# Performance work log

Measured on AMD Instinct MI355X. Metric: run time of the kernel, lower is better.

## Reference

```python
import jax, jax.numpy as jnp
import numpy as np

N_USER = 200000
N_ITEM = 100000
N = N_USER + N_ITEM
D = 64
NNZ = 1250000
B = 4096
N_LAYERS = 3


def setup_inputs() -> dict:
    key = jax.random.key(0)
    ks = jax.random.split(key, 7)
    user_emb = jax.random.normal(ks[0], (N_USER, D), dtype=jnp.float32) * 0.1
    item_emb = jax.random.normal(ks[1], (N_ITEM, D), dtype=jnp.float32) * 0.1
    # normalized-adjacency-like values (D^-1/2 A D^-1/2 entries are small positive)
    adj_val = jax.random.uniform(ks[2], (NNZ,), dtype=jnp.float32) * 0.1
    adj_row = jax.random.randint(ks[3], (NNZ,), 0, N, dtype=jnp.int32)
    adj_col = jax.random.randint(ks[4], (NNZ,), 0, N, dtype=jnp.int32)
    users = jax.random.randint(ks[5], (B,), 0, N_USER, dtype=jnp.int64)
    items = jax.random.randint(ks[6], (B,), 0, N_ITEM, dtype=jnp.int64)
    return {"user_emb": user_emb, "item_emb": item_emb, "adj_val": adj_val,
            "adj_row": adj_row, "adj_col": adj_col, "users": users, "items": items}


def reference(user_emb, item_emb, adj_val, adj_row, adj_col, users, items):
    # computer(): repeated SpMM propagation + mean over layer embeddings
    all_emb = jnp.concatenate([user_emb, item_emb], axis=0)  # [N, D]
    emb = all_emb
    acc = all_emb  # running sum of per-layer embeddings (fused stack+mean)
    for _ in range(N_LAYERS):
        # SpMM: out[r] += val * emb[c] for each edge (r, c)
        gathered = emb[adj_col] * adj_val[:, None]          # [NNZ, D]
        emb = jax.ops.segment_sum(gathered, adj_row, num_segments=N)
        acc = acc + emb
    light_out = acc / (N_LAYERS + 1)                        # mean over L+1 layers
    users_emb = light_out[users]                            # [B, D]
    items_emb = light_out[N_USER + items]                   # [B, D]
    # forward(): sigmoid(U @ I^T)
    return jax.nn.sigmoid(jnp.einsum('bd,cd->bc', users_emb, items_emb))
```

## Files before the change

### kernel.cpp

```cpp
#include <hip/hip_runtime.h>

#define N_USER 200000
#define N_ITEM 100000
#define NN     (N_USER + N_ITEM)
#define D      64
#define NNZ    1250000
#define B      4096

#define CHUNK  4096
#define NCHK   ((NNZ + CHUNK - 1) / CHUNK)
#define NBKT   ((NN + 1023) >> 10)
#define CAP    5000

#define VAL_SCALE   81920.0f
#define VAL_INV     (1.0f / 81920.0f)

typedef __attribute__((ext_vector_type(8))) short  short8;
typedef __attribute__((ext_vector_type(4))) float  f32x4;

__device__ __forceinline__ unsigned f2bf(float f) {
    unsigned u = __float_as_uint(f);
    return (u + 0x7fffu + ((u >> 16) & 1u)) >> 16;
}
__device__ __forceinline__ unsigned pack2(float lo, float hi) {
    return f2bf(lo) | (f2bf(hi) << 16);
}
__device__ __forceinline__ float bflo(unsigned u) { return __uint_as_float(u << 16); }
__device__ __forceinline__ float bfhi(unsigned u) { return __uint_as_float(u & 0xffff0000u); }

__global__ __launch_bounds__(256) void k_ui_init(const float4* __restrict__ user_emb,
                                                 const float4* __restrict__ item_emb,
                                                 const int* __restrict__ users,
                                                 const int* __restrict__ items,
                                                 float4* __restrict__ U,
                                                 float4* __restrict__ I) {
    int idx = blockIdx.x * 256 + threadIdx.x;
    if (idx >= 2 * B * 16) return;
    if (idx < B * 16) {
        int b = idx >> 4, q = idx & 15;
        U[idx] = user_emb[users[b] * 16 + q];
    } else {
        int j = idx - B * 16;
        int b = j >> 4, q = j & 15;
        I[j] = item_emb[items[b] * 16 + q];
    }
}

__global__ __launch_bounds__(256) void k_bhist(const int* __restrict__ adj_row,
                                               int* __restrict__ cntG) {
    __shared__ int c[NBKT];
    int t = threadIdx.x;
    for (int i = t; i < NBKT; i += 256) c[i] = 0;
    __syncthreads();
    int base = blockIdx.x * CHUNK;
    int n = min(CHUNK, NNZ - base);
    for (int i = t; i < n; i += 256) atomicAdd(&c[adj_row[base + i] >> 10], 1);
    __syncthreads();
    for (int i = t; i < NBKT; i += 256)
        if (c[i]) atomicAdd(&cntG[i], c[i]);
}

__global__ __launch_bounds__(512) void k_bscan(const int* __restrict__ cntG,
                                               int* __restrict__ bases,
                                               int* __restrict__ cursor,
                                               int* __restrict__ ptr) {
    __shared__ int s[512];
    int t = threadIdx.x;
    int v = (t < NBKT) ? cntG[t] : 0;
    s[t] = v;
    __syncthreads();
    for (int off = 1; off < 512; off <<= 1) {
        int x = (t >= off) ? s[t - off] : 0;
        __syncthreads();
        s[t] += x;
        __syncthreads();
    }
    if (t < NBKT) { bases[t] = s[t] - v; cursor[t] = s[t] - v; }
    if (t == 0) ptr[NN] = NNZ;
}

__global__ __launch_bounds__(256) void k_bin(const int* __restrict__ adj_row,
                                             const int* __restrict__ adj_col,
                                             const float* __restrict__ adj_val,
                                             int* __restrict__ cursor,
                                             uint2* __restrict__ binned) {
    __shared__ int cnt[NBKT], exc[NBKT], gof[NBKT], cur[NBKT];
    __shared__ int s[512];
    __shared__ uint2 stg[CHUNK];
    int t = threadIdx.x;
    int base = blockIdx.x * CHUNK;
    int n = min(CHUNK, NNZ - base);

    for (int i = t; i < NBKT; i += 256) cnt[i] = 0;
    __syncthreads();
    for (int i = t; i < n; i += 256) atomicAdd(&cnt[adj_row[base + i] >> 10], 1);
    __syncthreads();

    s[t]       = (t < NBKT) ? cnt[t] : 0;
    s[t + 256] = (t + 256 < NBKT) ? cnt[t + 256] : 0;
    __syncthreads();
    for (int off = 1; off < 512; off <<= 1) {
        int a  = (t >= off) ? s[t - off] : 0;
        int b2 = (t + 256 >= off) ? s[t + 256 - off] : 0;
        __syncthreads();
        s[t] += a; s[t + 256] += b2;
        __syncthreads();
    }
    for (int i = t; i < NBKT; i += 256) {
        int e = s[i] - cnt[i];
        exc[i] = e;
        cur[i] = e;
        gof[i] = cnt[i] ? atomicAdd(&cursor[i], cnt[i]) : 0;
    }
    __syncthreads();

    for (int i = t; i < n; i += 256) {
        int row = adj_row[base + i];
        int b2 = row >> 10;
        unsigned q = (unsigned)__float2int_rn(adj_val[base + i] * VAL_SCALE);
        if (q > 8191u) q = 8191u;
        unsigned cv = ((unsigned)adj_col[base + i] << 13) | q;
        int p = atomicAdd(&cur[b2], 1);
        stg[p] = make_uint2(cv, (unsigned)row);
    }
    __syncthreads();

    for (int i = t; i < n; i += 256) {
        uint2 e = stg[i];
        int b2 = (int)(e.y >> 10);
        binned[gof[b2] + (i - exc[b2])] = e;
    }
}

__global__ __launch_bounds__(1024) void k_fine(const int* __restrict__ bases,
                                               const int* __restrict__ cursor,
                                               const uint2* __restrict__ binned,
                                               int* __restrict__ ptr,
                                               unsigned* __restrict__ packed) {
    __shared__ int hist[1024], scn[1024];
    __shared__ unsigned img[CAP];
    int t = threadIdx.x;
    int b = blockIdx.x;
    int ebeg = bases[b], eend = cursor[b];
    int n = eend - ebeg;

    hist[t] = 0;
    __syncthreads();
    for (int i = t; i < n; i += 1024)
        atomicAdd(&hist[binned[ebeg + i].y & 1023], 1);
    __syncthreads();

    scn[t] = hist[t];
    __syncthreads();
    for (int off = 1; off < 1024; off <<= 1) {
        int a = (t >= off) ? scn[t - off] : 0;
        __syncthreads();
        scn[t] += a;
        __syncthreads();
    }
    int exc = scn[t] - hist[t];
    int row = (b << 10) + t;
    if (row < NN) ptr[row] = ebeg + exc;
    __syncthreads();
    scn[t] = exc;
    __syncthreads();

    for (int i = t; i < n; i += 1024) {
        uint2 e = binned[ebeg + i];
        int p = atomicAdd(&scn[e.y & 1023], 1);
        img[p] = e.x;
    }
    __syncthreads();
    for (int i = t; i < n; i += 1024) packed[ebeg + i] = img[i];
}

__global__ __launch_bounds__(256) void k_mark3(const int* __restrict__ users,
                                               const int* __restrict__ items,
                                               const int* __restrict__ ptr,
                                               const unsigned* __restrict__ packed,
                                               int* __restrict__ flags2,
                                               int* __restrict__ flags1) {
    int i = blockIdx.x * 256 + threadIdx.x;
    if (i >= 2 * B) return;
    int node = (i < B) ? users[i] : N_USER + items[i - B];
    flags2[node] = 1;
    flags1[node] = 1;
    int beg = ptr[node], end = ptr[node + 1];
    for (int e = beg; e < end; e++) flags2[(int)(packed[e] >> 13)] = 1;
}

__global__ __launch_bounds__(256) void k_mark2(const int* __restrict__ list2,
                                               const int* __restrict__ pn2,
                                               const int* __restrict__ ptr,
                                               const unsigned* __restrict__ packed,
                                               int* __restrict__ flags1) {
    int i = blockIdx.x * 256 + threadIdx.x;
    if (i >= pn2[0]) return;
    int row = list2[i];
    int beg = ptr[row], end = ptr[row + 1];
    for (int e = beg; e < end; e++) flags1[(int)(packed[e] >> 13)] = 1;
}

__global__ __launch_bounds__(256) void k_fcnt(const int* __restrict__ flags,
                                              int* __restrict__ cnts) {
    __shared__ int s[256];
    int t = threadIdx.x;
    int base = blockIdx.x * 1024 + t * 4;
    int c = 0;
#pragma unroll
    for (int i = 0; i < 4; i++) {
        int idx = base + i;
        if (idx < NN) c += flags[idx];
    }
    s[t] = c;
    __syncthreads();
    for (int off = 128; off > 0; off >>= 1) {
        if (t < off) s[t] += s[t + off];
        __syncthreads();
    }
    if (t == 0) cnts[blockIdx.x] = s[0];
}

__global__ __launch_bounds__(512) void k_fscan(const int* __restrict__ cnts,
                                               int* __restrict__ cbase,
                                               int* __restrict__ pn) {
    __shared__ int s[512];
    int t = threadIdx.x;
    int v = (t < NBKT) ? cnts[t] : 0;
    s[t] = v;
    __syncthreads();
    for (int off = 1; off < 512; off <<= 1) {
        int x = (t >= off) ? s[t - off] : 0;
        __syncthreads();
        s[t] += x;
        __syncthreads();
    }
    if (t < NBKT) cbase[t] = s[t] - v;
    if (t == 511) pn[0] = s[511];
}

__global__ __launch_bounds__(256) void k_fscat(const int* __restrict__ flags,
                                               const int* __restrict__ cbase,
                                               int* __restrict__ list) {
    __shared__ int s[256];
    int t = threadIdx.x;
    int base = blockIdx.x * 1024 + t * 4;
    int f[4];
    int c = 0;
#pragma unroll
    for (int i = 0; i < 4; i++) {
        int idx = base + i;
        f[i] = (idx < NN) ? flags[idx] : 0;
        c += f[i];
    }
    s[t] = c;
    __syncthreads();
    for (int off = 1; off < 256; off <<= 1) {
        int x = (t >= off) ? s[t - off] : 0;
        __syncthreads();
        s[t] += x;
        __syncthreads();
    }
    int run = cbase[blockIdx.x] + s[t] - c;
#pragma unroll
    for (int i = 0; i < 4; i++) {
        if (f[i]) list[run++] = base + i;
    }
}

template <bool L0>
__global__ __launch_bounds__(256) void k_spmm_list(const int* __restrict__ ptr,
                                                   const unsigned* __restrict__ packed,
                                                   const int* __restrict__ list,
                                                   const int* __restrict__ pn,
                                                   const float4* __restrict__ ue,
                                                   const float4* __restrict__ ie,
                                                   const uint4* __restrict__ ecur,
                                                   uint4* __restrict__ enext) {
    int t = blockIdx.x * 256 + threadIdx.x;
    int ir = t >> 3;
    if (ir >= pn[0]) return;
    int row = list[ir], q = t & 7;
    int beg = ptr[row], end = ptr[row + 1];
    float acc[8] = {};
    for (int i = beg; i < end; i++) {
        unsigned w = packed[i];
        int col = (int)(w >> 13);
        float val = (float)(w & 8191u) * VAL_INV;
        if (L0) {
            const float4* src = (col < N_USER) ? (ue + (size_t)col * 16)
                                               : (ie + (size_t)(col - N_USER) * 16);
            float4 a = src[q * 2];
            float4 b = src[q * 2 + 1];
            acc[0] += val * a.x; acc[1] += val * a.y;
            acc[2] += val * a.z; acc[3] += val * a.w;
            acc[4] += val * b.x; acc[5] += val * b.y;
            acc[6] += val * b.z; acc[7] += val * b.w;
        } else {
            uint4 u = ecur[(size_t)col * 8 + q];
            acc[0] += val * bflo(u.x); acc[1] += val * bfhi(u.x);
            acc[2] += val * bflo(u.y); acc[3] += val * bfhi(u.y);
            acc[4] += val * bflo(u.z); acc[5] += val * bfhi(u.z);
            acc[6] += val * bflo(u.w); acc[7] += val * bfhi(u.w);
        }
    }
    uint4 o;
    o.x = pack2(acc[0], acc[1]);
    o.y = pack2(acc[2], acc[3]);
    o.z = pack2(acc[4], acc[5]);
    o.w = pack2(acc[6], acc[7]);
    enext[(size_t)row * 8 + q] = o;
}

__global__ __launch_bounds__(256) void k_spmm_final(const int* __restrict__ ptr,
                                                    const unsigned* __restrict__ packed,
                                                    const int* __restrict__ users,
                                                    const int* __restrict__ items,
                                                    const uint4* __restrict__ ecur,
                                                    float4* __restrict__ U,
                                                    float4* __restrict__ I) {
    int idx = blockIdx.x * 256 + threadIdx.x;
    if (idx >= 2 * B * 8) return;
    int b = idx >> 3, q = idx & 7;
    int node;
    float4* dst;
    if (b < B) { node = users[b]; dst = U + idx * 2; }
    else       { node = N_USER + items[b - B]; dst = I + (idx - B * 8) * 2; }
    int beg = ptr[node], end = ptr[node + 1];
    float acc[8] = {};
    for (int i = beg; i < end; i++) {
        unsigned w = packed[i];
        int col = (int)(w >> 13);
        float val = (float)(w & 8191u) * VAL_INV;
        uint4 u = ecur[(size_t)col * 8 + q];
        acc[0] += val * bflo(u.x); acc[1] += val * bfhi(u.x);
        acc[2] += val * bflo(u.y); acc[3] += val * bfhi(u.y);
        acc[4] += val * bflo(u.z); acc[5] += val * bfhi(u.z);
        acc[6] += val * bflo(u.w); acc[7] += val * bfhi(u.w);
    }
    float4 lo = dst[0], hi = dst[1];
    lo.x += acc[0]; lo.y += acc[1]; lo.z += acc[2]; lo.w += acc[3];
    hi.x += acc[4]; hi.y += acc[5]; hi.z += acc[6]; hi.w += acc[7];
    dst[0] = lo; dst[1] = hi;
}

__global__ __launch_bounds__(256) void k_gather(const uint4* __restrict__ enext,
                                                const int* __restrict__ users,
                                                const int* __restrict__ items,
                                                float4* __restrict__ U,
                                                float4* __restrict__ I) {
    int idx = blockIdx.x * 256 + threadIdx.x;
    if (idx >= 2 * B * 8) return;
    int node;
    float4* dst;
    if (idx < B * 8) {
        int b = idx >> 3;
        node = users[b];
        dst = U + idx * 2;
    } else {
        int j = idx - B * 8;
        int b = j >> 3;
        node = N_USER + items[b];
        dst = I + j * 2;
    }
    int q = idx & 7;
    uint4 u = enext[(size_t)node * 8 + q];
    float4 lo = dst[0], hi = dst[1];
    lo.x += bflo(u.x); lo.y += bfhi(u.x);
    lo.z += bflo(u.y); lo.w += bfhi(u.y);
    hi.x += bflo(u.z); hi.y += bfhi(u.z);
    hi.z += bflo(u.w); hi.w += bfhi(u.w);
    dst[0] = lo; dst[1] = hi;
}

__global__ __launch_bounds__(256) void k_cvt(const float4* __restrict__ U,
                                             const float4* __restrict__ I,
                                             uint4* __restrict__ ubi) {
    int idx = blockIdx.x * 256 + threadIdx.x;
    if (idx >= 2 * B * 8) return;
    const float4* src = (idx < B * 8) ? (U + idx * 2) : (I + (idx - B * 8) * 2);
    float4 a = src[0], b = src[1];
    uint4 o;
    o.x = pack2(a.x, a.y);
    o.y = pack2(a.z, a.w);
    o.z = pack2(b.x, b.y);
    o.w = pack2(b.z, b.w);
    ubi[idx] = o;
}

__global__ __launch_bounds__(256) void k_gemm_mfma(const short8* __restrict__ ubi,
                                                   float* __restrict__ out) {
    __shared__ float lds[4 * 64 * 32];
    int t = threadIdx.x;
    int lane = t & 63;
    int w = t >> 6;
    int bx = blockIdx.x & 63;
    int by = blockIdx.x >> 6;
    int wm = (w >> 1) * 64;
    int wn = (w & 1) * 32;

    int r16  = lane & 15;
    int kg   = lane >> 4;

    short8 a[4][2], b[2][2];
#pragma unroll
    for (int mi = 0; mi < 4; mi++) {
        int row = by * 128 + wm + mi * 16 + r16;
#pragma unroll
        for (int kk = 0; kk < 2; kk++)
            a[mi][kk] = ubi[row * 8 + kk * 4 + kg];
    }
#pragma unroll
    for (int ni = 0; ni < 2; ni++) {
        int row = B + bx * 64 + wn + ni * 16 + r16;
#pragma unroll
        for (int kk = 0; kk < 2; kk++)
            b[ni][kk] = ubi[row * 8 + kk * 4 + kg];
    }

    f32x4 acc[4][2] = {};
#pragma unroll
    for (int mi = 0; mi < 4; mi++)
#pragma unroll
        for (int ni = 0; ni < 2; ni++) {
            acc[mi][ni] = __builtin_amdgcn_mfma_f32_16x16x32_bf16(
                a[mi][0], b[ni][0], acc[mi][ni], 0, 0, 0);
            acc[mi][ni] = __builtin_amdgcn_mfma_f32_16x16x32_bf16(
                a[mi][1], b[ni][1], acc[mi][ni], 0, 0, 0);
        }

    const float s = 1.0f / 16.0f;
    float* wls = lds + w * (64 * 32);
#pragma unroll
    for (int mi = 0; mi < 4; mi++) {
#pragma unroll
        for (int ni = 0; ni < 2; ni++) {
            int c  = ni * 16 + r16;
            int c4 = c >> 2, cl = c & 3;
#pragma unroll
            for (int r = 0; r < 4; r++) {
                int rr = mi * 16 + kg * 4 + r;
                float v = 1.0f / (1.0f + __expf(-acc[mi][ni][r] * s));
                wls[rr * 32 + (((c4 ^ (rr & 7)) << 2) | cl)] = v;
            }
        }
    }

    float4* out4 = (float4*)out;
    int j = lane & 7;
    int i0 = lane >> 3;
    size_t colbase = (size_t)(bx * 16) + (w & 1) * 8 + j;
#pragma unroll
    for (int iter = 0; iter < 8; iter++) {
        int i = iter * 8 + i0;
        float4 vv = *(float4*)&wls[i * 32 + ((j ^ (i & 7)) << 2)];
        out4[(size_t)(by * 128 + wm + i) * 1024 + colbase] = vv;
    }
}

extern "C" void kernel_launch(void* const* d_in, const int* in_sizes, int n_in,
                              void* d_out, int out_size, void* d_ws, size_t ws_size,
                              hipStream_t stream) {
    const float* user_emb = (const float*)d_in[0];
    const float* item_emb = (const float*)d_in[1];
    const float* adj_val  = (const float*)d_in[2];
    const int*   adj_row  = (const int*)d_in[3];
    const int*   adj_col  = (const int*)d_in[4];
    const int*   users    = (const int*)d_in[5];
    const int*   items    = (const int*)d_in[6];
    float* out = (float*)d_out;

    unsigned short* embA = (unsigned short*)d_ws;
    unsigned short* embB = embA + (size_t)NN * D;
    float* U    = (float*)(embB + (size_t)NN * D);
    float* I    = U + (size_t)B * D;
    int*   ptr  = (int*)(I + (size_t)B * D);
    unsigned* packed = (unsigned*)(ptr + (NN + 4));
    uint2* binned = (uint2*)(packed + NNZ);
    int*   cntG   = (int*)(binned + NNZ);
    int*   bases  = cntG + 512;
    int*   cursor = bases + 512;
    int*   cnts   = cursor + 512;
    int*   cbase  = cnts + 512;
    int*   pn     = cbase + 512;
    int*   flags2 = pn + 8;
    int*   flags1 = flags2 + NN;
    int*   list2  = flags1 + NN;
    int*   list1  = list2 + NN;
    unsigned short* ubi = (unsigned short*)(list1 + NN);

    k_ui_init<<<(2 * B * 16 + 255) / 256, 256, 0, stream>>>(
        (const float4*)user_emb, (const float4*)item_emb,
        users, items, (float4*)U, (float4*)I);

    hipMemsetAsync(cntG, 0, 512 * 4, stream);
    k_bhist<<<NCHK, 256, 0, stream>>>(adj_row, cntG);
    k_bscan<<<1, 512, 0, stream>>>(cntG, bases, cursor, ptr);
    k_bin<<<NCHK, 256, 0, stream>>>(adj_row, adj_col, adj_val, cursor, binned);
    k_fine<<<NBKT, 1024, 0, stream>>>(bases, cursor, binned, ptr, packed);

    hipMemsetAsync(flags2, 0, (size_t)2 * NN * 4, stream);
    k_mark3<<<(2 * B + 255) / 256, 256, 0, stream>>>(
        users, items, ptr, packed, flags2, flags1);
    k_fcnt<<<NBKT, 256, 0, stream>>>(flags2, cnts);
    k_fscan<<<1, 512, 0, stream>>>(cnts, cbase, &pn[0]);
    k_fscat<<<NBKT, 256, 0, stream>>>(flags2, cbase, list2);
    k_mark2<<<(NN + 255) / 256, 256, 0, stream>>>(list2, &pn[0], ptr, packed, flags1);
    k_fcnt<<<NBKT, 256, 0, stream>>>(flags1, cnts);
    k_fscan<<<1, 512, 0, stream>>>(cnts, cbase, &pn[1]);
    k_fscat<<<NBKT, 256, 0, stream>>>(flags1, cbase, list1);

    const int spmmGrid = (NN * 8 + 255) / 256;
    const int gatGrid  = (2 * B * 8 + 255) / 256;

    k_spmm_list<true><<<spmmGrid, 256, 0, stream>>>(
        ptr, packed, list1, &pn[1],
        (const float4*)user_emb, (const float4*)item_emb,
        (const uint4*)embA, (uint4*)embA);
    k_gather<<<gatGrid, 256, 0, stream>>>(
        (const uint4*)embA, users, items, (float4*)U, (float4*)I);

    k_spmm_list<false><<<spmmGrid, 256, 0, stream>>>(
        ptr, packed, list2, &pn[0],
        (const float4*)user_emb, (const float4*)item_emb,
        (const uint4*)embA, (uint4*)embB);
    k_gather<<<gatGrid, 256, 0, stream>>>(
        (const uint4*)embB, users, items, (float4*)U, (float4*)I);

    k_spmm_final<<<gatGrid, 256, 0, stream>>>(
        ptr, packed, users, items, (const uint4*)embB, (float4*)U, (float4*)I);

    k_cvt<<<(2 * B * 8 + 255) / 256, 256, 0, stream>>>(
        (const float4*)U, (const float4*)I, (uint4*)ubi);
    k_gemm_mfma<<<2048, 256, 0, stream>>>((const short8*)ubi, out);
}
```

Baseline: 159.3 us.

## Mark reachable rows on COO first and build CSR only for needed rows

Reachability marking (seed nodes, then two hops) now runs directly on the COO edge list with byte flags, before the CSR is built. Histogramming and binning then keep only edges whose row is in the two-hop set, which shrinks the binned and packed arrays. The flag count/scan/scatter kernels are replaced by atomic list compaction fused into the bucket-scan kernel. The gather, accumulate and convert kernels are merged into one finalize kernel. Layer 0 gets a 16-lane SpMM reading fp32 inputs, and the GEMM is split into two launches with nontemporal output stores. The price is two extra full passes over the edges and list ordering that depends on atomics.

```diff
diff --git a/kernel.cpp b/kernel.cpp
--- a/kernel.cpp
+++ b/kernel.cpp
@@ -15,6 +15,7 @@
 #define VAL_SCALE   81920.0f
 #define VAL_INV     (1.0f / 81920.0f)
 
+typedef unsigned char u8;
 typedef __attribute__((ext_vector_type(8))) short  short8;
 typedef __attribute__((ext_vector_type(4))) float  f32x4;
 
@@ -28,25 +29,30 @@
 __device__ __forceinline__ float bflo(unsigned u) { return __uint_as_float(u << 16); }
 __device__ __forceinline__ float bfhi(unsigned u) { return __uint_as_float(u & 0xffff0000u); }
 
-__global__ __launch_bounds__(256) void k_ui_init(const float4* __restrict__ user_emb,
-                                                 const float4* __restrict__ item_emb,
-                                                 const int* __restrict__ users,
-                                                 const int* __restrict__ items,
-                                                 float4* __restrict__ U,
-                                                 float4* __restrict__ I) {
-    int idx = blockIdx.x * 256 + threadIdx.x;
-    if (idx >= 2 * B * 16) return;
-    if (idx < B * 16) {
-        int b = idx >> 4, q = idx & 15;
-        U[idx] = user_emb[users[b] * 16 + q];
-    } else {
-        int j = idx - B * 16;
-        int b = j >> 4, q = j & 15;
-        I[j] = item_emb[items[b] * 16 + q];
-    }
+__global__ __launch_bounds__(256) void k_mark_sel(const int* __restrict__ users,
+                                                  const int* __restrict__ items,
+                                                  u8* __restrict__ flagS,
+                                                  u8* __restrict__ flag2,
+                                                  u8* __restrict__ flag1) {
+    int i = blockIdx.x * 256 + threadIdx.x;
+    if (i >= 2 * B) return;
+    int node = (i < B) ? users[i] : N_USER + items[i - B];
+    flagS[node] = 1;
+    flag2[node] = 1;
+    flag1[node] = 1;
+}
+
+__global__ __launch_bounds__(256) void k_markstep(const int* __restrict__ adj_row,
+                                                  const int* __restrict__ adj_col,
+                                                  const u8* __restrict__ flagIn,
+                                                  u8* __restrict__ flagOut) {
+    int e = blockIdx.x * 256 + threadIdx.x;
+    if (e >= NNZ) return;
+    if (flagIn[adj_row[e]]) flagOut[adj_col[e]] = 1;
 }
 
 __global__ __launch_bounds__(256) void k_bhist(const int* __restrict__ adj_row,
+                                               const u8* __restrict__ flag1,
                                                int* __restrict__ cntG) {
     __shared__ int c[NBKT];
     int t = threadIdx.x;
@@ -54,38 +60,59 @@
     __syncthreads();
     int base = blockIdx.x * CHUNK;
     int n = min(CHUNK, NNZ - base);
-    for (int i = t; i < n; i += 256) atomicAdd(&c[adj_row[base + i] >> 10], 1);
+    for (int i = t; i < n; i += 256) {
+        int r = adj_row[base + i];
+        if (flag1[r]) atomicAdd(&c[r >> 10], 1);
+    }
     __syncthreads();
     for (int i = t; i < NBKT; i += 256)
         if (c[i]) atomicAdd(&cntG[i], c[i]);
 }
 
-__global__ __launch_bounds__(512) void k_bscan(const int* __restrict__ cntG,
-                                               int* __restrict__ bases,
-                                               int* __restrict__ cursor,
-                                               int* __restrict__ ptr) {
-    __shared__ int s[512];
+__global__ __launch_bounds__(512) void k_scan_compact(const int* __restrict__ cntG,
+                                                      int* __restrict__ bases,
+                                                      int* __restrict__ cursor,
+                                                      int* __restrict__ ptr,
+                                                      const u8* __restrict__ flag2,
+                                                      const u8* __restrict__ flag1,
+                                                      int* __restrict__ list2,
+                                                      int* __restrict__ list1,
+                                                      int* __restrict__ pn) {
     int t = threadIdx.x;
-    int v = (t < NBKT) ? cntG[t] : 0;
-    s[t] = v;
-    __syncthreads();
-    for (int off = 1; off < 512; off <<= 1) {
-        int x = (t >= off) ? s[t - off] : 0;
+    if (blockIdx.x == 0) {
+        __shared__ int s[512];
+        int v = (t < NBKT) ? cntG[t] : 0;
+        s[t] = v;
         __syncthreads();
-        s[t] += x;
-        __syncthreads();
-    }
-    if (t < NBKT) { bases[t] = s[t] - v; cursor[t] = s[t] - v; }
-    if (t == 0) ptr[NN] = NNZ;
+        for (int off = 1; off < 512; off <<= 1) {
+            int x = (t >= off) ? s[t - off] : 0;
+            __syncthreads();
+            s[t] += x;
+            __syncthreads();
+        }
+        if (t < NBKT) { bases[t] = s[t] - v; cursor[t] = s[t] - v; }
+        if (t == NBKT - 1) ptr[NN] = s[t];
+    }
+    int base = blockIdx.x * 1024;
+#pragma unroll
+    for (int k = 0; k < 2; k++) {
+        int i = base + k * 512 + t;
+        if (i < NN) {
+            if (flag2[i]) list2[atomicAdd(&pn[0], 1)] = i;
+            if (flag1[i]) list1[atomicAdd(&pn[1], 1)] = i;
+        }
+    }
 }
 
 __global__ __launch_bounds__(256) void k_bin(const int* __restrict__ adj_row,
                                              const int* __restrict__ adj_col,
                                              const float* __restrict__ adj_val,
+                                             const u8* __restrict__ flag1,
                                              int* __restrict__ cursor,
                                              uint2* __restrict__ binned) {
     __shared__ int cnt[NBKT], exc[NBKT], gof[NBKT], cur[NBKT];
     __shared__ int s[512];
+    __shared__ int tot;
     __shared__ uint2 stg[CHUNK];
     int t = threadIdx.x;
     int base = blockIdx.x * CHUNK;
@@ -93,7 +120,10 @@
 
     for (int i = t; i < NBKT; i += 256) cnt[i] = 0;
     __syncthreads();
-    for (int i = t; i < n; i += 256) atomicAdd(&cnt[adj_row[base + i] >> 10], 1);
+    for (int i = t; i < n; i += 256) {
+        int r = adj_row[base + i];
+        if (flag1[r]) atomicAdd(&cnt[r >> 10], 1);
+    }
     __syncthreads();
 
     s[t]       = (t < NBKT) ? cnt[t] : 0;
@@ -112,20 +142,21 @@
         cur[i] = e;
         gof[i] = cnt[i] ? atomicAdd(&cursor[i], cnt[i]) : 0;
     }
+    if (t == 0) tot = s[NBKT - 1];
     __syncthreads();
 
     for (int i = t; i < n; i += 256) {
         int row = adj_row[base + i];
-        int b2 = row >> 10;
+        if (!flag1[row]) continue;
         unsigned q = (unsigned)__float2int_rn(adj_val[base + i] * VAL_SCALE);
         if (q > 8191u) q = 8191u;
         unsigned cv = ((unsigned)adj_col[base + i] << 13) | q;
-        int p = atomicAdd(&cur[b2], 1);
+        int p = atomicAdd(&cur[row >> 10], 1);
         stg[p] = make_uint2(cv, (unsigned)row);
     }
     __syncthreads();
 
-    for (int i = t; i < n; i += 256) {
+    for (int i = t; i < tot; i += 256) {
         uint2 e = stg[i];
         int b2 = (int)(e.y >> 10);
         binned[gof[b2] + (i - exc[b2])] = e;
@@ -174,109 +205,39 @@
     for (int i = t; i < n; i += 1024) packed[ebeg + i] = img[i];
 }
 
-__global__ __launch_bounds__(256) void k_mark3(const int* __restrict__ users,
-                                               const int* __restrict__ items,
-                                               const int* __restrict__ ptr,
+__global__ __launch_bounds__(256) void k_spmm16(const int* __restrict__ ptr,
+                                                const unsigned* __restrict__ packed,
+                                                const int* __restrict__ list,
+                                                const int* __restrict__ pn,
+                                                const float4* __restrict__ ue,
+                                                const float4* __restrict__ ie,
+                                                uint2* __restrict__ enext) {
+    int t = blockIdx.x * 256 + threadIdx.x;
+    int ir = t >> 4;
+    if (ir >= pn[1]) return;
+    int row = list[ir], q = t & 15;
+    int beg = ptr[row], end = ptr[row + 1];
+    float a0 = 0.f, a1 = 0.f, a2 = 0.f, a3 = 0.f;
+    for (int i = beg; i < end; i++) {
+        unsigned w = packed[i];
+        int col = (int)(w >> 13);
+        float val = (float)(w & 8191u) * VAL_INV;
+        float4 v = (col < N_USER) ? ue[(size_t)col * 16 + q]
+                                  : ie[(size_t)(col - N_USER) * 16 + q];
+        a0 += val * v.x; a1 += val * v.y; a2 += val * v.z; a3 += val * v.w;
+    }
+    uint2 o;
+    o.x = pack2(a0, a1);
+    o.y = pack2(a2, a3);
+    enext[(size_t)row * 16 + q] = o;
+}
+
+__global__ __launch_bounds__(256) void k_spmm8(const int* __restrict__ ptr,
                                                const unsigned* __restrict__ packed,
-                                               int* __restrict__ flags2,
-                                               int* __restrict__ flags1) {
-    int i = blockIdx.x * 256 + threadIdx.x;
-    if (i >= 2 * B) return;
-    int node = (i < B) ? users[i] : N_USER + items[i - B];
-    flags2[node] = 1;
-    flags1[node] = 1;
-    int beg = ptr[node], end = ptr[node + 1];
-    for (int e = beg; e < end; e++) flags2[(int)(packed[e] >> 13)] = 1;
-}
-
-__global__ __launch_bounds__(256) void k_mark2(const int* __restrict__ list2,
-                                               const int* __restrict__ pn2,
-                                               const int* __restrict__ ptr,
-                                               const unsigned* __restrict__ packed,
-                                               int* __restrict__ flags1) {
-    int i = blockIdx.x * 256 + threadIdx.x;
-    if (i >= pn2[0]) return;
-    int row = list2[i];
-    int beg = ptr[row], end = ptr[row + 1];
-    for (int e = beg; e < end; e++) flags1[(int)(packed[e] >> 13)] = 1;
-}
-
-__global__ __launch_bounds__(256) void k_fcnt(const int* __restrict__ flags,
-                                              int* __restrict__ cnts) {
-    __shared__ int s[256];
-    int t = threadIdx.x;
-    int base = blockIdx.x * 1024 + t * 4;
-    int c = 0;
-#pragma unroll
-    for (int i = 0; i < 4; i++) {
-        int idx = base + i;
-        if (idx < NN) c += flags[idx];
-    }
-    s[t] = c;
-    __syncthreads();
-    for (int off = 128; off > 0; off >>= 1) {
-        if (t < off) s[t] += s[t + off];
-        __syncthreads();
-    }
-    if (t == 0) cnts[blockIdx.x] = s[0];
-}
-
-__global__ __launch_bounds__(512) void k_fscan(const int* __restrict__ cnts,
-                                               int* __restrict__ cbase,
-                                               int* __restrict__ pn) {
-    __shared__ int s[512];
-    int t = threadIdx.x;
-    int v = (t < NBKT) ? cnts[t] : 0;
-    s[t] = v;
-    __syncthreads();
-    for (int off = 1; off < 512; off <<= 1) {
-        int x = (t >= off) ? s[t - off] : 0;
-        __syncthreads();
-        s[t] += x;
-        __syncthreads();
-    }
-    if (t < NBKT) cbase[t] = s[t] - v;
-    if (t == 511) pn[0] = s[511];
-}
-
-__global__ __launch_bounds__(256) void k_fscat(const int* __restrict__ flags,
-                                               const int* __restrict__ cbase,
-                                               int* __restrict__ list) {
-    __shared__ int s[256];
-    int t = threadIdx.x;
-    int base = blockIdx.x * 1024 + t * 4;
-    int f[4];
-    int c = 0;
-#pragma unroll
-    for (int i = 0; i < 4; i++) {
-        int idx = base + i;
-        f[i] = (idx < NN) ? flags[idx] : 0;
-        c += f[i];
-    }
-    s[t] = c;
-    __syncthreads();
-    for (int off = 1; off < 256; off <<= 1) {
-        int x = (t >= off) ? s[t - off] : 0;
-        __syncthreads();
-        s[t] += x;
-        __syncthreads();
-    }
-    int run = cbase[blockIdx.x] + s[t] - c;
-#pragma unroll
-    for (int i = 0; i < 4; i++) {
-        if (f[i]) list[run++] = base + i;
-    }
-}
-
-template <bool L0>
-__global__ __launch_bounds__(256) void k_spmm_list(const int* __restrict__ ptr,
-                                                   const unsigned* __restrict__ packed,
-                                                   const int* __restrict__ list,
-                                                   const int* __restrict__ pn,
-                                                   const float4* __restrict__ ue,
-                                                   const float4* __restrict__ ie,
-                                                   const uint4* __restrict__ ecur,
-                                                   uint4* __restrict__ enext) {
+                                               const int* __restrict__ list,
+                                               const int* __restrict__ pn,
+                                               const uint4* __restrict__ ecur,
+                                               uint4* __restrict__ enext) {
     int t = blockIdx.x * 256 + threadIdx.x;
     int ir = t >> 3;
     if (ir >= pn[0]) return;
@@ -287,22 +248,11 @@
         unsigned w = packed[i];
         int col = (int)(w >> 13);
         float val = (float)(w & 8191u) * VAL_INV;
-        if (L0) {
-            const float4* src = (col < N_USER) ? (ue + (size_t)col * 16)
-                                               : (ie + (size_t)(col - N_USER) * 16);
-            float4 a = src[q * 2];
-            float4 b = src[q * 2 + 1];
-            acc[0] += val * a.x; acc[1] += val * a.y;
-            acc[2] += val * a.z; acc[3] += val * a.w;
-            acc[4] += val * b.x; acc[5] += val * b.y;
-            acc[6] += val * b.z; acc[7] += val * b.w;
-        } else {
-            uint4 u = ecur[(size_t)col * 8 + q];
-            acc[0] += val * bflo(u.x); acc[1] += val * bfhi(u.x);
-            acc[2] += val * bflo(u.y); acc[3] += val * bfhi(u.y);
-            acc[4] += val * bflo(u.z); acc[5] += val * bfhi(u.z);
-            acc[6] += val * bflo(u.w); acc[7] += val * bfhi(u.w);
-        }
+        uint4 u = ecur[(size_t)col * 8 + q];
+        acc[0] += val * bflo(u.x); acc[1] += val * bfhi(u.x);
+        acc[2] += val * bflo(u.y); acc[3] += val * bfhi(u.y);
+        acc[4] += val * bflo(u.z); acc[5] += val * bfhi(u.z);
+        acc[6] += val * bflo(u.w); acc[7] += val * bfhi(u.w);
     }
     uint4 o;
     o.x = pack2(acc[0], acc[1]);
@@ -312,84 +262,55 @@
     enext[(size_t)row * 8 + q] = o;
 }
 
-__global__ __launch_bounds__(256) void k_spmm_final(const int* __restrict__ ptr,
-                                                    const unsigned* __restrict__ packed,
-                                                    const int* __restrict__ users,
-                                                    const int* __restrict__ items,
-                                                    const uint4* __restrict__ ecur,
-                                                    float4* __restrict__ U,
-                                                    float4* __restrict__ I) {
+__global__ __launch_bounds__(256) void k_finalize(const int* __restrict__ ptr,
+                                                  const unsigned* __restrict__ packed,
+                                                  const int* __restrict__ users,
+                                                  const int* __restrict__ items,
+                                                  const float4* __restrict__ ue,
+                                                  const float4* __restrict__ ie,
+                                                  const uint4* __restrict__ embA,
+                                                  const uint4* __restrict__ embB,
+                                                  uint4* __restrict__ ubi) {
     int idx = blockIdx.x * 256 + threadIdx.x;
     if (idx >= 2 * B * 8) return;
     int b = idx >> 3, q = idx & 7;
-    int node;
-    float4* dst;
-    if (b < B) { node = users[b]; dst = U + idx * 2; }
-    else       { node = N_USER + items[b - B]; dst = I + (idx - B * 8) * 2; }
+    int node = (b < B) ? users[b] : N_USER + items[b - B];
+    const float4* s0 = (node < N_USER) ? (ue + (size_t)node * 16)
+                                       : (ie + (size_t)(node - N_USER) * 16);
+    float4 x = s0[q * 2], y = s0[q * 2 + 1];
+    float acc[8] = {x.x, x.y, x.z, x.w, y.x, y.y, y.z, y.w};
+    uint4 ea = embA[(size_t)node * 8 + q];
+    acc[0] += bflo(ea.x); acc[1] += bfhi(ea.x);
+    acc[2] += bflo(ea.y); acc[3] += bfhi(ea.y);
+    acc[4] += bflo(ea.z); acc[5] += bfhi(ea.z);
+    acc[6] += bflo(ea.w); acc[7] += bfhi(ea.w);
+    uint4 eb = embB[(size_t)node * 8 + q];
+    acc[0] += bflo(eb.x); acc[1] += bfhi(eb.x);
+    acc[2] += bflo(eb.y); acc[3] += bfhi(eb.y);
+    acc[4] += bflo(eb.z); acc[5] += bfhi(eb.z);
+    acc[6] += bflo(eb.w); acc[7] += bfhi(eb.w);
     int beg = ptr[node], end = ptr[node + 1];
-    float acc[8] = {};
     for (int i = beg; i < end; i++) {
         unsigned w = packed[i];
         int col = (int)(w >> 13);
         float val = (float)(w & 8191u) * VAL_INV;
-        uint4 u = ecur[(size_t)col * 8 + q];
+        uint4 u = embB[(size_t)col * 8 + q];
         acc[0] += val * bflo(u.x); acc[1] += val * bfhi(u.x);
         acc[2] += val * bflo(u.y); acc[3] += val * bfhi(u.y);
         acc[4] += val * bflo(u.z); acc[5] += val * bfhi(u.z);
         acc[6] += val * bflo(u.w); acc[7] += val * bfhi(u.w);
     }
-    float4 lo = dst[0], hi = dst[1];
-    lo.x += acc[0]; lo.y += acc[1]; lo.z += acc[2]; lo.w += acc[3];
-    hi.x += acc[4]; hi.y += acc[5]; hi.z += acc[6]; hi.w += acc[7];
-    dst[0] = lo; dst[1] = hi;
-}
-
-__global__ __launch_bounds__(256) void k_gather(const uint4* __restrict__ enext,
-                                                const int* __restrict__ users,
-                                                const int* __restrict__ items,
-                                                float4* __restrict__ U,
-                                                float4* __restrict__ I) {
-    int idx = blockIdx.x * 256 + threadIdx.x;
-    if (idx >= 2 * B * 8) return;
-    int node;
-    float4* dst;
-    if (idx < B * 8) {
-        int b = idx >> 3;
-        node = users[b];
-        dst = U + idx * 2;
-    } else {
-        int j = idx - B * 8;
-        int b = j >> 3;
-        node = N_USER + items[b];
-        dst = I + j * 2;
-    }
-    int q = idx & 7;
-    uint4 u = enext[(size_t)node * 8 + q];
-    float4 lo = dst[0], hi = dst[1];
-    lo.x += bflo(u.x); lo.y += bfhi(u.x);
-    lo.z += bflo(u.y); lo.w += bfhi(u.y);
-    hi.x += bflo(u.z); hi.y += bfhi(u.z);
-    hi.z += bflo(u.w); hi.w += bfhi(u.w);
-    dst[0] = lo; dst[1] = hi;
-}
-
-__global__ __launch_bounds__(256) void k_cvt(const float4* __restrict__ U,
-                                             const float4* __restrict__ I,
-                                             uint4* __restrict__ ubi) {
-    int idx = blockIdx.x * 256 + threadIdx.x;
-    if (idx >= 2 * B * 8) return;
-    const float4* src = (idx < B * 8) ? (U + idx * 2) : (I + (idx - B * 8) * 2);
-    float4 a = src[0], b = src[1];
     uint4 o;
-    o.x = pack2(a.x, a.y);
-    o.y = pack2(a.z, a.w);
-    o.z = pack2(b.x, b.y);
-    o.w = pack2(b.z, b.w);
+    o.x = pack2(acc[0], acc[1]);
+    o.y = pack2(acc[2], acc[3]);
+    o.z = pack2(acc[4], acc[5]);
+    o.w = pack2(acc[6], acc[7]);
     ubi[idx] = o;
 }
 
 __global__ __launch_bounds__(256) void k_gemm_mfma(const short8* __restrict__ ubi,
-                                                   float* __restrict__ out) {
+                                                   float* __restrict__ out,
+                                                   int mbase) {
     __shared__ float lds[4 * 64 * 32];
     int t = threadIdx.x;
     int lane = t & 63;
@@ -398,14 +319,15 @@
     int by = blockIdx.x >> 6;
     int wm = (w >> 1) * 64;
     int wn = (w & 1) * 32;
-
-    int r16  = lane & 15;
-    int kg   = lane >> 4;
+    int mrow0 = mbase + by * 128;
+
+    int r16 = lane & 15;
+    int kg  = lane >> 4;
 
     short8 a[4][2], b[2][2];
 #pragma unroll
     for (int mi = 0; mi < 4; mi++) {
-        int row = by * 128 + wm + mi * 16 + r16;
+        int row = mrow0 + wm + mi * 16 + r16;
 #pragma unroll
         for (int kk = 0; kk < 2; kk++)
             a[mi][kk] = ubi[row * 8 + kk * 4 + kg];
@@ -446,15 +368,15 @@
         }
     }
 
-    float4* out4 = (float4*)out;
+    f32x4* out4 = (f32x4*)out;
     int j = lane & 7;
     int i0 = lane >> 3;
     size_t colbase = (size_t)(bx * 16) + (w & 1) * 8 + j;
 #pragma unroll
     for (int iter = 0; iter < 8; iter++) {
         int i = iter * 8 + i0;
-        float4 vv = *(float4*)&wls[i * 32 + ((j ^ (i & 7)) << 2)];
-        out4[(size_t)(by * 128 + wm + i) * 1024 + colbase] = vv;
+        f32x4 vv = *(f32x4*)&wls[i * 32 + ((j ^ (i & 7)) << 2)];
+        __builtin_nontemporal_store(vv, &out4[(size_t)(mrow0 + wm + i) * 1024 + colbase]);
     }
 }
 
@@ -472,65 +394,40 @@
 
     unsigned short* embA = (unsigned short*)d_ws;
     unsigned short* embB = embA + (size_t)NN * D;
-    float* U    = (float*)(embB + (size_t)NN * D);
-    float* I    = U + (size_t)B * D;
-    int*   ptr  = (int*)(I + (size_t)B * D);
+    int*   ptr    = (int*)(embB + (size_t)NN * D);
     unsigned* packed = (unsigned*)(ptr + (NN + 4));
     uint2* binned = (uint2*)(packed + NNZ);
-    int*   cntG   = (int*)(binned + NNZ);
-    int*   bases  = cntG + 512;
+    int*   bases  = (int*)(binned + NNZ);
     int*   cursor = bases + 512;
-    int*   cnts   = cursor + 512;
-    int*   cbase  = cnts + 512;
-    int*   pn     = cbase + 512;
-    int*   flags2 = pn + 8;
-    int*   flags1 = flags2 + NN;
-    int*   list2  = flags1 + NN;
+    int*   cntG   = cursor + 512;
+    int*   pn     = cntG + 512;
+    u8*    flagS  = (u8*)(pn + 8);
+    u8*    flag2  = flagS + NN;
+    u8*    flag1  = flag2 + NN;
+    const size_t zeroBytes = 512 * 4 + 8 * 4 + (size_t)3 * NN;
+    int*   list2  = (int*)(flag1 + NN);
     int*   list1  = list2 + NN;
     unsigned short* ubi = (unsigned short*)(list1 + NN);
 
-    k_ui_init<<<(2 * B * 16 + 255) / 256, 256, 0, stream>>>(
+    (void)hipMemsetAsync(cntG, 0, zeroBytes, stream);
+    k_mark_sel<<<(2 * B + 255) / 256, 256, 0, stream>>>(users, items, flagS, flag2, flag1);
+    k_markstep<<<(NNZ + 255) / 256, 256, 0, stream>>>(adj_row, adj_col, flagS, flag2);
+    k_markstep<<<(NNZ + 255) / 256, 256, 0, stream>>>(adj_row, adj_col, flag2, flag1);
+    k_bhist<<<NCHK, 256, 0, stream>>>(adj_row, flag1, cntG);
+    k_scan_compact<<<NBKT, 512, 0, stream>>>(cntG, bases, cursor, ptr,
+                                             flag2, flag1, list2, list1, pn);
+    k_bin<<<NCHK, 256, 0, stream>>>(adj_row, adj_col, adj_val, flag1, cursor, binned);
+    k_fine<<<NBKT, 1024, 0, stream>>>(bases, cursor, binned, ptr, packed);
+
+    k_spmm16<<<(NN * 16 + 255) / 256, 256, 0, stream>>>(
+        ptr, packed, list1, pn,
+        (const float4*)user_emb, (const float4*)item_emb, (uint2*)embA);
+    k_spmm8<<<(NN * 8 + 255) / 256, 256, 0, stream>>>(
+        ptr, packed, list2, pn, (const uint4*)embA, (uint4*)embB);
+    k_finalize<<<(2 * B * 8 + 255) / 256, 256, 0, stream>>>(
+        ptr, packed, users, items,
         (const float4*)user_emb, (const float4*)item_emb,
-        users, items, (float4*)U, (float4*)I);
-
-    hipMemsetAsync(cntG, 0, 512 * 4, stream);
-    k_bhist<<<NCHK, 256, 0, stream>>>(adj_row, cntG);
-    k_bscan<<<1, 512, 0, stream>>>(cntG, bases, cursor, ptr);
-    k_bin<<<NCHK, 256, 0, stream>>>(adj_row, adj_col, adj_val, cursor, binned);
-    k_fine<<<NBKT, 1024, 0, stream>>>(bases, cursor, binned, ptr, packed);
-
-    hipMemsetAsync(flags2, 0, (size_t)2 * NN * 4, stream);
-    k_mark3<<<(2 * B + 255) / 256, 256, 0, stream>>>(
-        users, items, ptr, packed, flags2, flags1);
-    k_fcnt<<<NBKT, 256, 0, stream>>>(flags2, cnts);
-    k_fscan<<<1, 512, 0, stream>>>(cnts, cbase, &pn[0]);
-    k_fscat<<<NBKT, 256, 0, stream>>>(flags2, cbase, list2);
-    k_mark2<<<(NN + 255) / 256, 256, 0, stream>>>(list2, &pn[0], ptr, packed, flags1);
-    k_fcnt<<<NBKT, 256, 0, stream>>>(flags1, cnts);
-    k_fscan<<<1, 512, 0, stream>>>(cnts, cbase, &pn[1]);
-    k_fscat<<<NBKT, 256, 0, stream>>>(flags1, cbase, list1);
-
-    const int spmmGrid = (NN * 8 + 255) / 256;
-    const int gatGrid  = (2 * B * 8 + 255) / 256;
-
-    k_spmm_list<true><<<spmmGrid, 256, 0, stream>>>(
-        ptr, packed, list1, &pn[1],
-        (const float4*)user_emb, (const float4*)item_emb,
-        (const uint4*)embA, (uint4*)embA);
-    k_gather<<<gatGrid, 256, 0, stream>>>(
-        (const uint4*)embA, users, items, (float4*)U, (float4*)I);
-
-    k_spmm_list<false><<<spmmGrid, 256, 0, stream>>>(
-        ptr, packed, list2, &pn[0],
-        (const float4*)user_emb, (const float4*)item_emb,
-        (const uint4*)embA, (uint4*)embB);
-    k_gather<<<gatGrid, 256, 0, stream>>>(
-        (const uint4*)embB, users, items, (float4*)U, (float4*)I);
-
-    k_spmm_final<<<gatGrid, 256, 0, stream>>>(
-        ptr, packed, users, items, (const uint4*)embB, (float4*)U, (float4*)I);
-
-    k_cvt<<<(2 * B * 8 + 255) / 256, 256, 0, stream>>>(
-        (const float4*)U, (const float4*)I, (uint4*)ubi);
-    k_gemm_mfma<<<2048, 256, 0, stream>>>((const short8*)ubi, out);
-}
+        (const uint4*)embA, (const uint4*)embB, (uint4*)ubi);
+    k_gemm_mfma<<<1024, 256, 0, stream>>>((const short8*)ubi, out, 0);
+    k_gemm_mfma<<<1024, 256, 0, stream>>>((const short8*)ubi, out, 2048);
+}
```

After: 264.2 us. 1.66x slower.
